# Optimization experiments

Measured on AMD Instinct MI355X. Metric: run time of the kernel, lower is better.

The kernel has to match this reference:

```python
import jax, jax.numpy as jnp
import numpy as np

N_NODES = 50000
N_EDGES = 800000
IN_DIM = 128
HID_DIM = 64
OUT_DIM = 40
N_REL = 8


def setup_inputs() -> dict:
    key = jax.random.key(0)
    ks = jax.random.split(key, 12)
    x = jax.random.normal(ks[0], (N_NODES, IN_DIM), dtype=jnp.float32)
    edge_index = jax.random.randint(ks[1], (2, N_EDGES), 0, N_NODES, dtype=jnp.int64)
    edge_type = jax.random.randint(ks[2], (N_EDGES,), 0, N_REL, dtype=jnp.int64)
    s = 0.05
    W1 = jax.random.normal(ks[3], (N_REL, IN_DIM, HID_DIM), dtype=jnp.float32) * s
    root1 = jax.random.normal(ks[4], (IN_DIM, HID_DIM), dtype=jnp.float32) * s
    b1 = jnp.zeros((HID_DIM,), dtype=jnp.float32)
    W2 = jax.random.normal(ks[5], (N_REL, HID_DIM, HID_DIM), dtype=jnp.float32) * s
    root2 = jax.random.normal(ks[6], (HID_DIM, HID_DIM), dtype=jnp.float32) * s
    b2 = jnp.zeros((HID_DIM,), dtype=jnp.float32)
    Wl = jax.random.normal(ks[7], (HID_DIM, OUT_DIM), dtype=jnp.float32) * s
    bl = jnp.zeros((OUT_DIM,), dtype=jnp.float32)
    return {"x": x, "edge_index": edge_index, "edge_type": edge_type,
            "W1": W1, "root1": root1, "b1": b1,
            "W2": W2, "root2": root2, "b2": b2,
            "Wl": Wl, "bl": bl}


def _rgcn_conv(x, W, Wroot, b, src, dst, edge_type):
    # PyG RGCNConv (no bases/blocks, aggr='mean'):
    #   out[i] = sum_r mean_{(j->i) of rel r} (x[j] @ W[r]) + x[i] @ Wroot + b
    N = x.shape[0]
    R = W.shape[0]
    h = jnp.einsum('ni,rio->rno', x, W)        # [R, N, out]
    msgs = h[edge_type, src]                   # [E, out] edge gather
    seg = edge_type * N + dst                  # per (relation, dst) segment
    sums = jax.ops.segment_sum(msgs, seg, num_segments=R * N)
    cnt = jax.ops.segment_sum(jnp.ones((msgs.shape[0],), x.dtype), seg,
                              num_segments=R * N)
    mean = sums / jnp.maximum(cnt, 1.0)[:, None]
    agg = mean.reshape(R, N, -1).sum(axis=0)   # sum over relations
    return agg + x @ Wroot + b


def reference(x, edge_index, edge_type, W1, root1, b1, W2, root2, b2, Wl, bl):
    src, dst = edge_index[0], edge_index[1]
    h = jax.nn.relu(_rgcn_conv(x, W1, root1, b1, src, dst, edge_type))
    # dropout is identity in eval mode
    h = jax.nn.relu(_rgcn_conv(h, W2, root2, b2, src, dst, edge_type))
    logits = h @ Wl + bl
    return jax.nn.log_softmax(logits, axis=1)
```

## Files before the change

kernel.cpp:

```cpp
#include <hip/hip_runtime.h>
#include <hip/hip_bf16.h>
#include <cmath>


#define IN_DIM 128
#define HID 64
#define OUT_DIM 40
#define NREL 8
#define NCOLS 576
#define CAP 64
#define CSTR 16

typedef __attribute__((ext_vector_type(8))) short short8;
typedef __attribute__((ext_vector_type(4))) short short4v;
typedef __attribute__((ext_vector_type(4))) float floatx4;
typedef __attribute__((ext_vector_type(2))) float f32x2;

static __device__ __forceinline__ short f2bf(float f) {
  __hip_bfloat16 h = __float2bfloat16(f);
  return __builtin_bit_cast(short, h);
}
static __device__ __forceinline__ float bflo(unsigned int u) {
  return __int_as_float(u << 16);
}
static __device__ __forceinline__ float bfhi(unsigned int u) {
  return __int_as_float(u & 0xffff0000u);
}
static __device__ __forceinline__ unsigned int packbf(float x, float y) {
  unsigned int lo = (unsigned short)f2bf(x);
  unsigned int hi = (unsigned short)f2bf(y);
  return lo | (hi << 16);
}

__global__ void pack_bt(const float* __restrict__ W1, const float* __restrict__ root1,
                        short* __restrict__ Bt1,
                        const float* __restrict__ W2, const float* __restrict__ root2,
                        short* __restrict__ Bt2,
                        int* __restrict__ cursor, int nzero4) {
  const int PB1 = (NCOLS * IN_DIM + 255) / 256;
  const int PB2 = (NCOLS * HID + 255) / 256;
  int b = blockIdx.x;
  if (b < PB1) {
    int i = b * 256 + threadIdx.x;
    if (i >= NCOLS * IN_DIM) return;
    int c = i / IN_DIM, k = i % IN_DIM;
    float v = (c < NREL * HID)
      ? W1[((size_t)(c >> 6) * IN_DIM + k) * HID + (c & 63)]
      : root1[(size_t)k * HID + (c - NREL * HID)];
    Bt1[i] = f2bf(v);
  } else if (b < PB1 + PB2) {
    int i = (b - PB1) * 256 + threadIdx.x;
    if (i >= NCOLS * HID) return;
    int c = i / HID, k = i % HID;
    float v = (c < NREL * HID)
      ? W2[((size_t)(c >> 6) * HID + k) * HID + (c & 63)]
      : root2[(size_t)k * HID + (c - NREL * HID)];
    Bt2[i] = f2bf(v);
  } else {
    int i = (b - PB1 - PB2) * 256 + threadIdx.x;
    if (i < nzero4) {
      int4 z; z.x = 0; z.y = 0; z.z = 0; z.w = 0;
      ((int4*)cursor)[i] = z;
    }
  }
}

template<int K, int AMODE>
__device__ __forceinline__ void gemm_dev(
    short* As, short* Bs,
    const void* __restrict__ Aptr, const short* __restrict__ Bt,
    const float* __restrict__ bias, short* __restrict__ H,
    unsigned short* __restrict__ AGG, int M, int row0)
{
  constexpr int AST = K + 8;
  int tid = threadIdx.x;
  int wv = tid >> 6, lane = tid & 63;
  int lm = lane & 15, quad = lane >> 4;

  if (AMODE == 0) {
    const float* A = (const float*)Aptr;
    constexpr int CH = K / 4;
    for (int i = tid; i < 64 * CH; i += 256) {
      int r = i / CH, kq = i % CH;
      int gr = row0 + r; if (gr >= M) gr = M - 1;
      float4 v = *(const float4*)(A + (unsigned)(gr * K + kq * 4));
      short4v s;
      s.x = f2bf(v.x); s.y = f2bf(v.y); s.z = f2bf(v.z); s.w = f2bf(v.w);
      *(short4v*)(As + r * AST + kq * 4) = s;
    }
  } else {
    const short* A = (const short*)Aptr;
    constexpr int CH = K / 8;
    for (int i = tid; i < 64 * CH; i += 256) {
      int r = i / CH, ko = i % CH;
      int gr = row0 + r; if (gr >= M) gr = M - 1;
      short8 v = *(const short8*)(A + (unsigned)(gr * K + ko * 8));
      #pragma unroll
      for (int j = 0; j < 8; ++j)
        if ((unsigned short)v[j] & 0x8000u) v[j] = 0;
      *(short8*)(As + r * AST + ko * 8) = v;
    }
  }

  const short* ap = As + (16 * wv + lm) * AST + quad * 8;

  for (int cy = 0; cy < 9; ++cy) {
    constexpr int CB = K / 8;
    for (int i = tid; i < 64 * CB; i += 256) {
      int n = i / CB, ko = i % CB;
      short8 v = *(const short8*)(Bt + (unsigned)((cy * 64 + n) * K + ko * 8));
      *(short8*)(Bs + n * AST + ko * 8) = v;
    }
    __syncthreads();

    floatx4 acc[4] = {{0,0,0,0},{0,0,0,0},{0,0,0,0},{0,0,0,0}};
    #pragma unroll
    for (int ks = 0; ks < K / 32; ++ks) {
      short8 a = *(const short8*)(ap + ks * 32);
      #pragma unroll
      for (int nb = 0; nb < 4; ++nb) {
        short8 b = *(const short8*)(Bs + (nb * 16 + lm) * AST + ks * 32 + quad * 8);
        acc[nb] = __builtin_amdgcn_mfma_f32_16x16x32_bf16(a, b, acc[nb], 0, 0, 0);
      }
    }
    __syncthreads();

    int mbase = row0 + 16 * wv + quad * 4;
    if (cy < 8) {
      #pragma unroll
      for (int nb = 0; nb < 4; ++nb) {
        int col = cy * 64 + nb * 16 + lm;
        #pragma unroll
        for (int r = 0; r < 4; ++r) {
          int mg = mbase + r;
          if (mg < M) H[(unsigned)mg * (NREL * HID) + col] = f2bf(acc[nb][r]);
        }
      }
    } else {
      #pragma unroll
      for (int nb = 0; nb < 4; ++nb) {
        int col = nb * 16 + lm;
        float bv = bias[col];
        #pragma unroll
        for (int r = 0; r < 4; ++r) {
          int mg = mbase + r;
          if (mg < M)
            AGG[(unsigned)mg * HID + col] = (unsigned short)f2bf(acc[nb][r] + bv);
        }
      }
    }
  }
}

__global__ __launch_bounds__(256, 4) void gemm1_scatter(
    const float* __restrict__ A, const short* __restrict__ Bt,
    const float* __restrict__ bias, short* __restrict__ H,
    unsigned short* __restrict__ AGG, int M, int GB,
    const int* __restrict__ src, const int* __restrict__ dst,
    const int* __restrict__ et,
    int* __restrict__ cursor, int* __restrict__ ev, int E)
{
  constexpr int AST = IN_DIM + 8;
  __shared__ short As[64 * AST];
  __shared__ short Bs[64 * AST];
  if ((int)blockIdx.x < GB) {
    gemm_dev<IN_DIM, 0>(As, Bs, A, Bt, bias, H, AGG, M, blockIdx.x * 64);
  } else {
    int e = (blockIdx.x - GB) * 256 + threadIdx.x;
    if (e >= E) return;
    int d = dst[e];
    int pos = atomicAdd(&cursor[d * CSTR], 1);
    if (pos < CAP)
      __builtin_nontemporal_store((src[e] << 3) | et[e], &ev[d * CAP + pos]);
  }
}

__global__ __launch_bounds__(256, 4) void gemm2_mfma(
    const unsigned short* __restrict__ A, const short* __restrict__ Bt,
    const float* __restrict__ bias, short* __restrict__ H,
    unsigned short* __restrict__ AGG, int M)
{
  constexpr int AST = HID + 8;
  __shared__ short As[64 * AST];
  __shared__ short Bs[64 * AST];
  gemm_dev<HID, 1>(As, Bs, A, Bt, bias, H, AGG, M, blockIdx.x * 64);
}

static __device__ __forceinline__ void agg_half2(
    const uint2* __restrict__ Hu2, const int* __restrict__ evrow,
    int cnt, int qloc, int sub, float wreg, int h,
    float& a0, float& a1, float& a2, float& a3)
{
  int npass = (cnt + 15) >> 4;
  f32x2 A01 = {a0, a1}, A23 = {a2, a3};
  for (int P = 0; P < npass; ++P) {
    const int4* pp = (const int4*)(evrow + P * 16 + qloc * 8);
    int4 v0 = pp[0], v1 = pp[1];
    int vv[8] = {v0.x, v0.y, v0.z, v0.w, v1.x, v1.y, v1.z, v1.w};
    int sb = P * 16 + qloc * 8;
    uint2 hv[8];
    float ww[8];
    #pragma unroll
    for (int i = 0; i < 8; ++i) {
      bool ok = (sb + i) < cnt;
      int v = ok ? vv[i] : 0;
      hv[i] = Hu2[(unsigned)v * 16u + (unsigned)sub];
      float w = __shfl(wreg, h * 32 + (v & 7), 64);
      ww[i] = ok ? w : 0.f;
    }
    #pragma unroll
    for (int i = 0; i < 8; ++i) {
      f32x2 w2 = {ww[i], ww[i]};
      f32x2 h01 = {bflo(hv[i].x), bfhi(hv[i].x)};
      f32x2 h23 = {bflo(hv[i].y), bfhi(hv[i].y)};
      A01 += h01 * w2;
      A23 += h23 * w2;
    }
  }
  a0 = A01.x; a1 = A01.y; a2 = A23.x; a3 = A23.y;
  a0 += __shfl_xor(a0, 16, 64);
  a1 += __shfl_xor(a1, 16, 64);
  a2 += __shfl_xor(a2, 16, 64);
  a3 += __shfl_xor(a3, 16, 64);
}

static __device__ __forceinline__ float rel_weight(
    const int* __restrict__ evr, int cnt, int lhl, int h)
{
  int e0 = evr[lhl], e1 = evr[lhl + 32];
  bool v0 = lhl < cnt, v1 = (lhl + 32) < cnt;
  int r0 = e0 & 7, r1 = e1 & 7;
  unsigned long long hm = 0xffffffffull << (h * 32);
  int myrel = lhl & 7;
  int c = 0;
  #pragma unroll
  for (int r = 0; r < 8; ++r) {
    unsigned long long m0 = __ballot(v0 && (r0 == r));
    unsigned long long m1 = __ballot(v1 && (r1 == r));
    int cr = __popcll(m0 & hm) + __popcll(m1 & hm);
    if (myrel == r) c = cr;
  }
  return (c > 0) ? (1.0f / (float)c) : 0.0f;
}

__global__ __launch_bounds__(256) void csr_agg(
    const short* __restrict__ H, const int* __restrict__ cursor,
    const int* __restrict__ ev, unsigned short* __restrict__ AGG, int N)
{
  int tid = threadIdx.x;
  int wv = tid >> 6, lane = tid & 63;
  int h = lane >> 5, lhl = lane & 31, qloc = lhl >> 4, sub = lhl & 15;
  int d = blockIdx.x * 8 + wv * 2 + h;
  int dc = d < N ? d : N - 1;

  int cnt = cursor[dc * CSTR]; if (cnt > CAP) cnt = CAP;
  const int* evr = ev + dc * CAP;
  float wreg = rel_weight(evr, cnt, lhl, h);

  float a0 = 0.f, a1 = 0.f, a2 = 0.f, a3 = 0.f;
  uint2* aggrow = (uint2*)(AGG + (size_t)dc * HID);
  if (qloc == 0) {
    uint2 iv = aggrow[sub];
    a0 = bflo(iv.x); a1 = bfhi(iv.x); a2 = bflo(iv.y); a3 = bfhi(iv.y);
  }
  agg_half2((const uint2*)H, evr, cnt, qloc, sub, wreg, h, a0, a1, a2, a3);
  if (d < N && qloc == 0) {
    uint2 ov;
    ov.x = packbf(a0, a1);
    ov.y = packbf(a2, a3);
    aggrow[sub] = ov;
  }
}

__global__ __launch_bounds__(256) void csr_agg_final(
    const short* __restrict__ H, const int* __restrict__ cursor,
    const int* __restrict__ ev, const unsigned short* __restrict__ AGG,
    const float* __restrict__ Wl, const float* __restrict__ bl,
    float* __restrict__ out, int N)
{
  __shared__ float sWl[HID * OUT_DIM];
  __shared__ float sbl[OUT_DIM];
  __shared__ float sh[8][HID];
  int tid = threadIdx.x;
  int wv = tid >> 6, lane = tid & 63;
  int h = lane >> 5, lhl = lane & 31, qloc = lhl >> 4, sub = lhl & 15;
  int d = blockIdx.x * 8 + wv * 2 + h;
  int dc = d < N ? d : N - 1;

  int cnt = cursor[dc * CSTR]; if (cnt > CAP) cnt = CAP;
  uint2 iv = ((const uint2*)(AGG + (size_t)dc * HID))[sub];
  const int* evr = ev + dc * CAP;
  float wreg = rel_weight(evr, cnt, lhl, h);

  for (int i = tid; i < HID * OUT_DIM; i += 256) sWl[i] = Wl[i];
  if (tid < OUT_DIM) sbl[tid] = bl[tid];
  __syncthreads();

  float a0 = 0.f, a1 = 0.f, a2 = 0.f, a3 = 0.f;
  if (qloc == 0) {
    a0 = bflo(iv.x); a1 = bfhi(iv.x); a2 = bflo(iv.y); a3 = bfhi(iv.y);
  }
  agg_half2((const uint2*)H, evr, cnt, qloc, sub, wreg, h, a0, a1, a2, a3);
  if (qloc == 0) {
    float4 v;
    v.x = fmaxf(a0, 0.f); v.y = fmaxf(a1, 0.f);
    v.z = fmaxf(a2, 0.f); v.w = fmaxf(a3, 0.f);
    *(float4*)(&sh[wv * 2 + h][4 * sub]) = v;
  }
  __syncthreads();

  #pragma unroll
  for (int ii = 0; ii < 2; ++ii) {
    int dd = blockIdx.x * 8 + wv * 2 + ii;
    const float* row = sh[wv * 2 + ii];
    float logit = -__builtin_inff();
    if (lane < OUT_DIM) {
      float t = sbl[lane];
      #pragma unroll 8
      for (int k = 0; k < HID; ++k) t += row[k] * sWl[k * OUT_DIM + lane];
      logit = t;
    }
    float m = logit;
    #pragma unroll
    for (int o = 32; o > 0; o >>= 1) m = fmaxf(m, __shfl_xor(m, o, 64));
    float ex = (lane < OUT_DIM) ? expf(logit - m) : 0.f;
    float s = ex;
    #pragma unroll
    for (int o = 32; o > 0; o >>= 1) s += __shfl_xor(s, o, 64);
    if (dd < N && lane < OUT_DIM)
      out[(size_t)dd * OUT_DIM + lane] = logit - m - logf(s);
  }
}

extern "C" void kernel_launch(void* const* d_in, const int* in_sizes, int n_in,
                              void* d_out, int out_size, void* d_ws, size_t ws_size,
                              hipStream_t stream) {
  const float* x     = (const float*)d_in[0];
  const int*   eidx  = (const int*)d_in[1];
  const int*   etype = (const int*)d_in[2];
  const float* W1    = (const float*)d_in[3];
  const float* root1 = (const float*)d_in[4];
  const float* b1    = (const float*)d_in[5];
  const float* W2    = (const float*)d_in[6];
  const float* root2 = (const float*)d_in[7];
  const float* b2    = (const float*)d_in[8];
  const float* Wl    = (const float*)d_in[9];
  const float* bl    = (const float*)d_in[10];

  int N = in_sizes[0] / IN_DIM;
  int E = in_sizes[2];
  const int* srcp = eidx;
  const int* dstp = eidx + E;

  char* ws = (char*)d_ws;
  size_t off = 0;
  auto alloc = [&](size_t bytes) -> char* {
    char* p = ws + off;
    off += (bytes + 255) & ~(size_t)255;
    return p;
  };
  short* Bt1    = (short*)alloc((size_t)NCOLS * IN_DIM * 2);
  short* Bt2    = (short*)alloc((size_t)NCOLS * HID * 2);
  int*   cursor = (int*)alloc((size_t)N * CSTR * 4);
  int*   ev     = (int*)alloc((size_t)N * CAP * 4);
  short* H1     = (short*)alloc((size_t)N * NREL * HID * 2);
  short* H2     = (short*)alloc((size_t)N * NREL * HID * 2);
  unsigned short* AGG1 = (unsigned short*)alloc((size_t)N * HID * 2);
  unsigned short* AGG2 = (unsigned short*)alloc((size_t)N * HID * 2);

  const int PB1 = (NCOLS * IN_DIM + 255) / 256;
  const int PB2 = (NCOLS * HID + 255) / 256;
  int nzero4 = (N * CSTR) / 4;
  int ZB = (nzero4 + 255) / 256;
  pack_bt<<<PB1 + PB2 + ZB, 256, 0, stream>>>(W1, root1, Bt1, W2, root2, Bt2,
                                              cursor, nzero4);

  int GB = (N + 63) / 64;
  int SB = (E + 255) / 256;
  gemm1_scatter<<<GB + SB, 256, 0, stream>>>(x, Bt1, b1, H1, AGG1, N, GB,
                                             srcp, dstp, etype, cursor, ev, E);

  csr_agg<<<(N + 7) / 8, 256, 0, stream>>>(H1, cursor, ev, AGG1, N);

  gemm2_mfma<<<GB, 256, 0, stream>>>(AGG1, Bt2, b2, H2, AGG2, N);

  csr_agg_final<<<(N + 7) / 8, 256, 0, stream>>>(H2, cursor, ev, AGG2,
                                                 Wl, bl, (float*)d_out, N);
}
```

Before: 217.1 us.

## Prefetch B tiles into registers, vectorize GEMM stores, split scatter kernel

```diff
diff --git a/kernel.cpp b/kernel.cpp
--- a/kernel.cpp
+++ b/kernel.cpp
@@ -65,6 +65,19 @@
   }
 }
 
+__global__ __launch_bounds__(256) void scatter_ev(
+    const int* __restrict__ src, const int* __restrict__ dst,
+    const int* __restrict__ et,
+    int* __restrict__ cursor, int* __restrict__ ev, int E)
+{
+  int e = blockIdx.x * 256 + threadIdx.x;
+  if (e >= E) return;
+  int d = dst[e];
+  int pos = atomicAdd(&cursor[d * CSTR], 1);
+  if (pos < CAP)
+    __builtin_nontemporal_store((src[e] << 3) | et[e], &ev[d * CAP + pos]);
+}
+
 template<int K, int AMODE>
 __device__ __forceinline__ void gemm_dev(
     short* As, short* Bs,
@@ -73,9 +86,23 @@
     unsigned short* __restrict__ AGG, int M, int row0)
 {
   constexpr int AST = K + 8;
+  constexpr int CB = K / 8;
+  constexpr int NCH = 64 * CB / 256;
   int tid = threadIdx.x;
   int wv = tid >> 6, lane = tid & 63;
   int lm = lane & 15, quad = lane >> 4;
+
+  int bn[NCH], bko[NCH];
+  #pragma unroll
+  for (int j = 0; j < NCH; ++j) {
+    int i = tid + j * 256;
+    bn[j] = i / CB; bko[j] = i % CB;
+  }
+
+  short8 breg[NCH];
+  #pragma unroll
+  for (int j = 0; j < NCH; ++j)
+    breg[j] = *(const short8*)(Bt + (unsigned)(bn[j] * K + bko[j] * 8));
 
   if (AMODE == 0) {
     const float* A = (const float*)Aptr;
@@ -103,15 +130,20 @@
   }
 
   const short* ap = As + (16 * wv + lm) * AST + quad * 8;
+  int rowg = row0 + 16 * wv + lm;
 
   for (int cy = 0; cy < 9; ++cy) {
-    constexpr int CB = K / 8;
-    for (int i = tid; i < 64 * CB; i += 256) {
-      int n = i / CB, ko = i % CB;
-      short8 v = *(const short8*)(Bt + (unsigned)((cy * 64 + n) * K + ko * 8));
-      *(short8*)(Bs + n * AST + ko * 8) = v;
-    }
+    #pragma unroll
+    for (int j = 0; j < NCH; ++j)
+      *(short8*)(Bs + bn[j] * AST + bko[j] * 8) = breg[j];
     __syncthreads();
+
+    if (cy < 8) {
+      #pragma unroll
+      for (int j = 0; j < NCH; ++j)
+        breg[j] = *(const short8*)(
+            Bt + (unsigned)(((cy + 1) * 64 + bn[j]) * K + bko[j] * 8));
+    }
 
     floatx4 acc[4] = {{0,0,0,0},{0,0,0,0},{0,0,0,0},{0,0,0,0}};
     #pragma unroll
@@ -120,59 +152,47 @@
       #pragma unroll
       for (int nb = 0; nb < 4; ++nb) {
         short8 b = *(const short8*)(Bs + (nb * 16 + lm) * AST + ks * 32 + quad * 8);
-        acc[nb] = __builtin_amdgcn_mfma_f32_16x16x32_bf16(a, b, acc[nb], 0, 0, 0);
+        acc[nb] = __builtin_amdgcn_mfma_f32_16x16x32_bf16(b, a, acc[nb], 0, 0, 0);
       }
     }
     __syncthreads();
 
-    int mbase = row0 + 16 * wv + quad * 4;
     if (cy < 8) {
-      #pragma unroll
-      for (int nb = 0; nb < 4; ++nb) {
-        int col = cy * 64 + nb * 16 + lm;
+      if (rowg < M) {
+        short* hrow = H + (unsigned)rowg * (NREL * HID) + cy * 64 + quad * 4;
         #pragma unroll
-        for (int r = 0; r < 4; ++r) {
-          int mg = mbase + r;
-          if (mg < M) H[(unsigned)mg * (NREL * HID) + col] = f2bf(acc[nb][r]);
+        for (int nb = 0; nb < 4; ++nb) {
+          short4v s;
+          s.x = f2bf(acc[nb][0]); s.y = f2bf(acc[nb][1]);
+          s.z = f2bf(acc[nb][2]); s.w = f2bf(acc[nb][3]);
+          *(short4v*)(hrow + nb * 16) = s;
         }
       }
     } else {
-      #pragma unroll
-      for (int nb = 0; nb < 4; ++nb) {
-        int col = nb * 16 + lm;
-        float bv = bias[col];
+      if (rowg < M) {
+        unsigned short* arow = AGG + (unsigned)rowg * HID + quad * 4;
         #pragma unroll
-        for (int r = 0; r < 4; ++r) {
-          int mg = mbase + r;
-          if (mg < M)
-            AGG[(unsigned)mg * HID + col] = (unsigned short)f2bf(acc[nb][r] + bv);
+        for (int nb = 0; nb < 4; ++nb) {
+          float4 bv = *(const float4*)(bias + nb * 16 + quad * 4);
+          short4v s;
+          s.x = f2bf(acc[nb][0] + bv.x); s.y = f2bf(acc[nb][1] + bv.y);
+          s.z = f2bf(acc[nb][2] + bv.z); s.w = f2bf(acc[nb][3] + bv.w);
+          *(short4v*)(arow + nb * 16) = s;
         }
       }
     }
   }
 }
 
-__global__ __launch_bounds__(256, 4) void gemm1_scatter(
+__global__ __launch_bounds__(256, 4) void gemm1_mfma(
     const float* __restrict__ A, const short* __restrict__ Bt,
     const float* __restrict__ bias, short* __restrict__ H,
-    unsigned short* __restrict__ AGG, int M, int GB,
-    const int* __restrict__ src, const int* __restrict__ dst,
-    const int* __restrict__ et,
-    int* __restrict__ cursor, int* __restrict__ ev, int E)
+    unsigned short* __restrict__ AGG, int M)
 {
   constexpr int AST = IN_DIM + 8;
   __shared__ short As[64 * AST];
   __shared__ short Bs[64 * AST];
-  if ((int)blockIdx.x < GB) {
-    gemm_dev<IN_DIM, 0>(As, Bs, A, Bt, bias, H, AGG, M, blockIdx.x * 64);
-  } else {
-    int e = (blockIdx.x - GB) * 256 + threadIdx.x;
-    if (e >= E) return;
-    int d = dst[e];
-    int pos = atomicAdd(&cursor[d * CSTR], 1);
-    if (pos < CAP)
-      __builtin_nontemporal_store((src[e] << 3) | et[e], &ev[d * CAP + pos]);
-  }
+  gemm_dev<IN_DIM, 0>(As, Bs, A, Bt, bias, H, AGG, M, blockIdx.x * 64);
 }
 
 __global__ __launch_bounds__(256, 4) void gemm2_mfma(
@@ -377,8 +397,9 @@
 
   int GB = (N + 63) / 64;
   int SB = (E + 255) / 256;
-  gemm1_scatter<<<GB + SB, 256, 0, stream>>>(x, Bt1, b1, H1, AGG1, N, GB,
-                                             srcp, dstp, etype, cursor, ev, E);
+  scatter_ev<<<SB, 256, 0, stream>>>(srcp, dstp, etype, cursor, ev, E);
+
+  gemm1_mfma<<<GB, 256, 0, stream>>>(x, Bt1, b1, H1, AGG1, N);
 
   csr_agg<<<(N + 7) / 8, 256, 0, stream>>>(H1, cursor, ev, AGG1, N);
 
```

Result: slower. 258.8 us (+19.2%).

## Aggregate-then-transform layer 2 with per-relation edge buckets

Applied to the files above, without the earlier changes.

```diff
diff --git a/kernel.cpp b/kernel.cpp
--- a/kernel.cpp
+++ b/kernel.cpp
@@ -8,13 +8,14 @@
 #define OUT_DIM 40
 #define NREL 8
 #define NCOLS 576
-#define CAP 64
+#define K2 576
+#define CAPR 32
+#define EVR 256
 #define CSTR 16
 
 typedef __attribute__((ext_vector_type(8))) short short8;
 typedef __attribute__((ext_vector_type(4))) short short4v;
 typedef __attribute__((ext_vector_type(4))) float floatx4;
-typedef __attribute__((ext_vector_type(2))) float f32x2;
 
 static __device__ __forceinline__ short f2bf(float f) {
   __hip_bfloat16 h = __float2bfloat16(f);
@@ -35,10 +36,10 @@
 __global__ void pack_bt(const float* __restrict__ W1, const float* __restrict__ root1,
                         short* __restrict__ Bt1,
                         const float* __restrict__ W2, const float* __restrict__ root2,
-                        short* __restrict__ Bt2,
+                        short* __restrict__ Bt2b,
                         int* __restrict__ cursor, int nzero4) {
   const int PB1 = (NCOLS * IN_DIM + 255) / 256;
-  const int PB2 = (NCOLS * HID + 255) / 256;
+  const int PB2 = (64 * K2 + 255) / 256;
   int b = blockIdx.x;
   if (b < PB1) {
     int i = b * 256 + threadIdx.x;
@@ -50,12 +51,12 @@
     Bt1[i] = f2bf(v);
   } else if (b < PB1 + PB2) {
     int i = (b - PB1) * 256 + threadIdx.x;
-    if (i >= NCOLS * HID) return;
-    int c = i / HID, k = i % HID;
-    float v = (c < NREL * HID)
-      ? W2[((size_t)(c >> 6) * HID + k) * HID + (c & 63)]
-      : root2[(size_t)k * HID + (c - NREL * HID)];
-    Bt2[i] = f2bf(v);
+    if (i >= 64 * K2) return;
+    int col = i / K2, kk = i % K2;
+    float v = (kk < NREL * HID)
+      ? W2[(size_t)kk * HID + col]
+      : root2[(size_t)(kk - NREL * HID) * HID + col];
+    Bt2b[i] = f2bf(v);
   } else {
     int i = (b - PB1 - PB2) * 256 + threadIdx.x;
     if (i < nzero4) {
@@ -65,20 +66,19 @@
   }
 }
 
-template<int K, int AMODE>
-__device__ __forceinline__ void gemm_dev(
+__device__ __forceinline__ void gemm1_body(
     short* As, short* Bs,
-    const void* __restrict__ Aptr, const short* __restrict__ Bt,
+    const float* __restrict__ A, const short* __restrict__ Bt,
     const float* __restrict__ bias, short* __restrict__ H,
     unsigned short* __restrict__ AGG, int M, int row0)
 {
+  constexpr int K = IN_DIM;
   constexpr int AST = K + 8;
   int tid = threadIdx.x;
   int wv = tid >> 6, lane = tid & 63;
   int lm = lane & 15, quad = lane >> 4;
 
-  if (AMODE == 0) {
-    const float* A = (const float*)Aptr;
+  {
     constexpr int CH = K / 4;
     for (int i = tid; i < 64 * CH; i += 256) {
       int r = i / CH, kq = i % CH;
@@ -87,18 +87,6 @@
       short4v s;
       s.x = f2bf(v.x); s.y = f2bf(v.y); s.z = f2bf(v.z); s.w = f2bf(v.w);
       *(short4v*)(As + r * AST + kq * 4) = s;
-    }
-  } else {
-    const short* A = (const short*)Aptr;
-    constexpr int CH = K / 8;
-    for (int i = tid; i < 64 * CH; i += 256) {
-      int r = i / CH, ko = i % CH;
-      int gr = row0 + r; if (gr >= M) gr = M - 1;
-      short8 v = *(const short8*)(A + (unsigned)(gr * K + ko * 8));
-      #pragma unroll
-      for (int j = 0; j < 8; ++j)
-        if ((unsigned short)v[j] & 0x8000u) v[j] = 0;
-      *(short8*)(As + r * AST + ko * 8) = v;
     }
   }
 
@@ -164,160 +152,163 @@
   __shared__ short As[64 * AST];
   __shared__ short Bs[64 * AST];
   if ((int)blockIdx.x < GB) {
-    gemm_dev<IN_DIM, 0>(As, Bs, A, Bt, bias, H, AGG, M, blockIdx.x * 64);
+    gemm1_body(As, Bs, A, Bt, bias, H, AGG, M, blockIdx.x * 64);
   } else {
     int e = (blockIdx.x - GB) * 256 + threadIdx.x;
     if (e >= E) return;
     int d = dst[e];
-    int pos = atomicAdd(&cursor[d * CSTR], 1);
-    if (pos < CAP)
-      __builtin_nontemporal_store((src[e] << 3) | et[e], &ev[d * CAP + pos]);
-  }
-}
-
-__global__ __launch_bounds__(256, 4) void gemm2_mfma(
-    const unsigned short* __restrict__ A, const short* __restrict__ Bt,
-    const float* __restrict__ bias, short* __restrict__ H,
-    unsigned short* __restrict__ AGG, int M)
-{
-  constexpr int AST = HID + 8;
+    int r = et[e];
+    int pos = atomicAdd(&cursor[d * CSTR + r], 1);
+    if (pos < CAPR)
+      __builtin_nontemporal_store(src[e], &ev[(d << 8) + (r << 5) + pos]);
+  }
+}
+
+__global__ __launch_bounds__(256) void csr_agg1(
+    const short* __restrict__ H1, const int* __restrict__ cursor,
+    const int* __restrict__ ev, unsigned short* __restrict__ h, int N)
+{
+  int tid = threadIdx.x;
+  int wv = tid >> 6, lane = tid & 63;
+  int rel = lane >> 3, dg = lane & 7;
+  int d = blockIdx.x * 4 + wv;
+
+  int cnt = cursor[d * CSTR + rel]; if (cnt > CAPR) cnt = CAPR;
+  const int* evg = ev + ((size_t)d << 8) + (rel << 5);
+  int evs = evg[dg];
+
+  float acc[8] = {0.f,0.f,0.f,0.f,0.f,0.f,0.f,0.f};
+  for (int s = 0; s < cnt; ++s) {
+    int srcj = (s < 8) ? __shfl(evs, (lane & 56) + s, 64) : evg[s];
+    uint4 hv = *(const uint4*)(H1 + ((size_t)srcj << 9) + (rel << 6) + (dg << 3));
+    acc[0] += bflo(hv.x); acc[1] += bfhi(hv.x);
+    acc[2] += bflo(hv.y); acc[3] += bfhi(hv.y);
+    acc[4] += bflo(hv.z); acc[5] += bfhi(hv.z);
+    acc[6] += bflo(hv.w); acc[7] += bfhi(hv.w);
+  }
+  float w = (cnt > 0) ? (1.0f / (float)cnt) : 0.0f;
+  #pragma unroll
+  for (int j = 0; j < 8; ++j) acc[j] *= w;
+  #pragma unroll
+  for (int off = 8; off <= 32; off <<= 1) {
+    #pragma unroll
+    for (int j = 0; j < 8; ++j) acc[j] += __shfl_xor(acc[j], off, 64);
+  }
+  if (rel == 0) {
+    unsigned short* hrow = h + (size_t)d * HID + (dg << 3);
+    uint4 sv = *(const uint4*)hrow;
+    float v0 = fmaxf(acc[0] + bflo(sv.x), 0.f);
+    float v1 = fmaxf(acc[1] + bfhi(sv.x), 0.f);
+    float v2 = fmaxf(acc[2] + bflo(sv.y), 0.f);
+    float v3 = fmaxf(acc[3] + bfhi(sv.y), 0.f);
+    float v4 = fmaxf(acc[4] + bflo(sv.z), 0.f);
+    float v5 = fmaxf(acc[5] + bfhi(sv.z), 0.f);
+    float v6 = fmaxf(acc[6] + bflo(sv.w), 0.f);
+    float v7 = fmaxf(acc[7] + bfhi(sv.w), 0.f);
+    uint4 ov;
+    ov.x = packbf(v0, v1); ov.y = packbf(v2, v3);
+    ov.z = packbf(v4, v5); ov.w = packbf(v6, v7);
+    *(uint4*)hrow = ov;
+  }
+}
+
+__global__ __launch_bounds__(256) void agg2(
+    const unsigned short* __restrict__ h, const int* __restrict__ cursor,
+    const int* __restrict__ ev, short* __restrict__ m2, int N)
+{
+  int tid = threadIdx.x;
+  int wv = tid >> 6, lane = tid & 63;
+  int rel = lane >> 3, dg = lane & 7;
+  int d = blockIdx.x * 4 + wv;
+
+  int cnt = cursor[d * CSTR + rel]; if (cnt > CAPR) cnt = CAPR;
+  const int* evg = ev + ((size_t)d << 8) + (rel << 5);
+  int evs = evg[dg];
+
+  float acc[8] = {0.f,0.f,0.f,0.f,0.f,0.f,0.f,0.f};
+  for (int s = 0; s < cnt; ++s) {
+    int srcj = (s < 8) ? __shfl(evs, (lane & 56) + s, 64) : evg[s];
+    uint4 hv = *(const uint4*)(h + ((size_t)srcj << 6) + (dg << 3));
+    acc[0] += bflo(hv.x); acc[1] += bfhi(hv.x);
+    acc[2] += bflo(hv.y); acc[3] += bfhi(hv.y);
+    acc[4] += bflo(hv.z); acc[5] += bfhi(hv.z);
+    acc[6] += bflo(hv.w); acc[7] += bfhi(hv.w);
+  }
+  float w = (cnt > 0) ? (1.0f / (float)cnt) : 0.0f;
+  uint4 ov;
+  ov.x = packbf(acc[0] * w, acc[1] * w);
+  ov.y = packbf(acc[2] * w, acc[3] * w);
+  ov.z = packbf(acc[4] * w, acc[5] * w);
+  ov.w = packbf(acc[6] * w, acc[7] * w);
+  *(uint4*)(m2 + (size_t)d * K2 + (rel << 6) + (dg << 3)) = ov;
+  if (rel == 0) {
+    uint4 hv = *(const uint4*)(h + ((size_t)d << 6) + (dg << 3));
+    *(uint4*)(m2 + (size_t)d * K2 + 512 + (dg << 3)) = hv;
+  }
+}
+
+__global__ __launch_bounds__(256) void gemm2c(
+    const short* __restrict__ m2, const short* __restrict__ Bt2b,
+    const float* __restrict__ b2, const float* __restrict__ Wl,
+    const float* __restrict__ bl, float* __restrict__ out, int N)
+{
+  constexpr int AST = 64 + 8;
   __shared__ short As[64 * AST];
   __shared__ short Bs[64 * AST];
-  gemm_dev<HID, 1>(As, Bs, A, Bt, bias, H, AGG, M, blockIdx.x * 64);
-}
-
-static __device__ __forceinline__ void agg_half2(
-    const uint2* __restrict__ Hu2, const int* __restrict__ evrow,
-    int cnt, int qloc, int sub, float wreg, int h,
-    float& a0, float& a1, float& a2, float& a3)
-{
-  int npass = (cnt + 15) >> 4;
-  f32x2 A01 = {a0, a1}, A23 = {a2, a3};
-  for (int P = 0; P < npass; ++P) {
-    const int4* pp = (const int4*)(evrow + P * 16 + qloc * 8);
-    int4 v0 = pp[0], v1 = pp[1];
-    int vv[8] = {v0.x, v0.y, v0.z, v0.w, v1.x, v1.y, v1.z, v1.w};
-    int sb = P * 16 + qloc * 8;
-    uint2 hv[8];
-    float ww[8];
-    #pragma unroll
-    for (int i = 0; i < 8; ++i) {
-      bool ok = (sb + i) < cnt;
-      int v = ok ? vv[i] : 0;
-      hv[i] = Hu2[(unsigned)v * 16u + (unsigned)sub];
-      float w = __shfl(wreg, h * 32 + (v & 7), 64);
-      ww[i] = ok ? w : 0.f;
-    }
-    #pragma unroll
-    for (int i = 0; i < 8; ++i) {
-      f32x2 w2 = {ww[i], ww[i]};
-      f32x2 h01 = {bflo(hv[i].x), bfhi(hv[i].x)};
-      f32x2 h23 = {bflo(hv[i].y), bfhi(hv[i].y)};
-      A01 += h01 * w2;
-      A23 += h23 * w2;
-    }
-  }
-  a0 = A01.x; a1 = A01.y; a2 = A23.x; a3 = A23.y;
-  a0 += __shfl_xor(a0, 16, 64);
-  a1 += __shfl_xor(a1, 16, 64);
-  a2 += __shfl_xor(a2, 16, 64);
-  a3 += __shfl_xor(a3, 16, 64);
-}
-
-static __device__ __forceinline__ float rel_weight(
-    const int* __restrict__ evr, int cnt, int lhl, int h)
-{
-  int e0 = evr[lhl], e1 = evr[lhl + 32];
-  bool v0 = lhl < cnt, v1 = (lhl + 32) < cnt;
-  int r0 = e0 & 7, r1 = e1 & 7;
-  unsigned long long hm = 0xffffffffull << (h * 32);
-  int myrel = lhl & 7;
-  int c = 0;
-  #pragma unroll
-  for (int r = 0; r < 8; ++r) {
-    unsigned long long m0 = __ballot(v0 && (r0 == r));
-    unsigned long long m1 = __ballot(v1 && (r1 == r));
-    int cr = __popcll(m0 & hm) + __popcll(m1 & hm);
-    if (myrel == r) c = cr;
-  }
-  return (c > 0) ? (1.0f / (float)c) : 0.0f;
-}
-
-__global__ __launch_bounds__(256) void csr_agg(
-    const short* __restrict__ H, const int* __restrict__ cursor,
-    const int* __restrict__ ev, unsigned short* __restrict__ AGG, int N)
-{
+  __shared__ float sz[64][64];
+  __shared__ float sWl[HID * OUT_DIM];
+  __shared__ float sbl[OUT_DIM];
   int tid = threadIdx.x;
   int wv = tid >> 6, lane = tid & 63;
-  int h = lane >> 5, lhl = lane & 31, qloc = lhl >> 4, sub = lhl & 15;
-  int d = blockIdx.x * 8 + wv * 2 + h;
-  int dc = d < N ? d : N - 1;
-
-  int cnt = cursor[dc * CSTR]; if (cnt > CAP) cnt = CAP;
-  const int* evr = ev + dc * CAP;
-  float wreg = rel_weight(evr, cnt, lhl, h);
-
-  float a0 = 0.f, a1 = 0.f, a2 = 0.f, a3 = 0.f;
-  uint2* aggrow = (uint2*)(AGG + (size_t)dc * HID);
-  if (qloc == 0) {
-    uint2 iv = aggrow[sub];
-    a0 = bflo(iv.x); a1 = bfhi(iv.x); a2 = bflo(iv.y); a3 = bfhi(iv.y);
-  }
-  agg_half2((const uint2*)H, evr, cnt, qloc, sub, wreg, h, a0, a1, a2, a3);
-  if (d < N && qloc == 0) {
-    uint2 ov;
-    ov.x = packbf(a0, a1);
-    ov.y = packbf(a2, a3);
-    aggrow[sub] = ov;
-  }
-}
-
-__global__ __launch_bounds__(256) void csr_agg_final(
-    const short* __restrict__ H, const int* __restrict__ cursor,
-    const int* __restrict__ ev, const unsigned short* __restrict__ AGG,
-    const float* __restrict__ Wl, const float* __restrict__ bl,
-    float* __restrict__ out, int N)
-{
-  __shared__ float sWl[HID * OUT_DIM];
-  __shared__ float sbl[OUT_DIM];
-  __shared__ float sh[8][HID];
-  int tid = threadIdx.x;
-  int wv = tid >> 6, lane = tid & 63;
-  int h = lane >> 5, lhl = lane & 31, qloc = lhl >> 4, sub = lhl & 15;
-  int d = blockIdx.x * 8 + wv * 2 + h;
-  int dc = d < N ? d : N - 1;
-
-  int cnt = cursor[dc * CSTR]; if (cnt > CAP) cnt = CAP;
-  uint2 iv = ((const uint2*)(AGG + (size_t)dc * HID))[sub];
-  const int* evr = ev + dc * CAP;
-  float wreg = rel_weight(evr, cnt, lhl, h);
+  int lm = lane & 15, quad = lane >> 4;
+  int row0 = blockIdx.x * 64;
 
   for (int i = tid; i < HID * OUT_DIM; i += 256) sWl[i] = Wl[i];
   if (tid < OUT_DIM) sbl[tid] = bl[tid];
-  __syncthreads();
-
-  float a0 = 0.f, a1 = 0.f, a2 = 0.f, a3 = 0.f;
-  if (qloc == 0) {
-    a0 = bflo(iv.x); a1 = bfhi(iv.x); a2 = bflo(iv.y); a3 = bfhi(iv.y);
-  }
-  agg_half2((const uint2*)H, evr, cnt, qloc, sub, wreg, h, a0, a1, a2, a3);
-  if (qloc == 0) {
-    float4 v;
-    v.x = fmaxf(a0, 0.f); v.y = fmaxf(a1, 0.f);
-    v.z = fmaxf(a2, 0.f); v.w = fmaxf(a3, 0.f);
-    *(float4*)(&sh[wv * 2 + h][4 * sub]) = v;
-  }
-  __syncthreads();
+
+  floatx4 acc[4] = {{0,0,0,0},{0,0,0,0},{0,0,0,0},{0,0,0,0}};
+  for (int kt = 0; kt < 9; ++kt) {
+    #pragma unroll
+    for (int j = 0; j < 2; ++j) {
+      int i = tid + j * 256;
+      int r = i >> 3, ch = i & 7;
+      int gr = row0 + r; if (gr >= N) gr = N - 1;
+      *(short8*)(As + r * AST + ch * 8) =
+          *(const short8*)(m2 + (size_t)gr * K2 + kt * 64 + ch * 8);
+      *(short8*)(Bs + r * AST + ch * 8) =
+          *(const short8*)(Bt2b + (unsigned)(r * K2 + kt * 64 + ch * 8));
+    }
+    __syncthreads();
+    #pragma unroll
+    for (int ks = 0; ks < 2; ++ks) {
+      short8 a = *(const short8*)(As + (16 * wv + lm) * AST + ks * 32 + quad * 8);
+      #pragma unroll
+      for (int nb = 0; nb < 4; ++nb) {
+        short8 b = *(const short8*)(Bs + (nb * 16 + lm) * AST + ks * 32 + quad * 8);
+        acc[nb] = __builtin_amdgcn_mfma_f32_16x16x32_bf16(a, b, acc[nb], 0, 0, 0);
+      }
+    }
+    __syncthreads();
+  }
 
   #pragma unroll
-  for (int ii = 0; ii < 2; ++ii) {
-    int dd = blockIdx.x * 8 + wv * 2 + ii;
-    const float* row = sh[wv * 2 + ii];
+  for (int nb = 0; nb < 4; ++nb) {
+    int col = nb * 16 + lm;
+    float bv = b2[col];
+    #pragma unroll
+    for (int r = 0; r < 4; ++r)
+      sz[16 * wv + quad * 4 + r][col] = fmaxf(acc[nb][r] + bv, 0.f);
+  }
+
+  for (int rr = 0; rr < 16; ++rr) {
+    int row = 16 * wv + rr;
+    int dd = row0 + row;
+    const float* zr = sz[row];
     float logit = -__builtin_inff();
     if (lane < OUT_DIM) {
       float t = sbl[lane];
       #pragma unroll 8
-      for (int k = 0; k < HID; ++k) t += row[k] * sWl[k * OUT_DIM + lane];
+      for (int k = 0; k < HID; ++k) t += zr[k] * sWl[k * OUT_DIM + lane];
       logit = t;
     }
     float m = logit;
@@ -360,19 +351,19 @@
     return p;
   };
   short* Bt1    = (short*)alloc((size_t)NCOLS * IN_DIM * 2);
-  short* Bt2    = (short*)alloc((size_t)NCOLS * HID * 2);
+  short* Bt2b   = (short*)alloc((size_t)64 * K2 * 2);
   int*   cursor = (int*)alloc((size_t)N * CSTR * 4);
-  int*   ev     = (int*)alloc((size_t)N * CAP * 4);
-  short* H1     = (short*)alloc((size_t)N * NREL * HID * 2);
-  short* H2     = (short*)alloc((size_t)N * NREL * HID * 2);
+  int*   ev     = (int*)alloc((size_t)N * EVR * 4);
+  char*  h1m2   = alloc((size_t)N * K2 * 2);
+  short* H1     = (short*)h1m2;
+  short* m2     = (short*)h1m2;
   unsigned short* AGG1 = (unsigned short*)alloc((size_t)N * HID * 2);
-  unsigned short* AGG2 = (unsigned short*)alloc((size_t)N * HID * 2);
 
   const int PB1 = (NCOLS * IN_DIM + 255) / 256;
-  const int PB2 = (NCOLS * HID + 255) / 256;
+  const int PB2 = (64 * K2 + 255) / 256;
   int nzero4 = (N * CSTR) / 4;
   int ZB = (nzero4 + 255) / 256;
-  pack_bt<<<PB1 + PB2 + ZB, 256, 0, stream>>>(W1, root1, Bt1, W2, root2, Bt2,
+  pack_bt<<<PB1 + PB2 + ZB, 256, 0, stream>>>(W1, root1, Bt1, W2, root2, Bt2b,
                                               cursor, nzero4);
 
   int GB = (N + 63) / 64;
@@ -380,10 +371,9 @@
   gemm1_scatter<<<GB + SB, 256, 0, stream>>>(x, Bt1, b1, H1, AGG1, N, GB,
                                              srcp, dstp, etype, cursor, ev, E);
 
-  csr_agg<<<(N + 7) / 8, 256, 0, stream>>>(H1, cursor, ev, AGG1, N);
-
-  gemm2_mfma<<<GB, 256, 0, stream>>>(AGG1, Bt2, b2, H2, AGG2, N);
-
-  csr_agg_final<<<(N + 7) / 8, 256, 0, stream>>>(H2, cursor, ev, AGG2,
-                                                 Wl, bl, (float*)d_out, N);
-}
+  csr_agg1<<<N / 4, 256, 0, stream>>>(H1, cursor, ev, AGG1, N);
+
+  agg2<<<N / 4, 256, 0, stream>>>(AGG1, cursor, ev, m2, N);
+
+  gemm2c<<<GB, 256, 0, stream>>>(m2, Bt2b, b2, Wl, bl, (float*)d_out, N);
+}
```

After: 263.0 us. 21.2% more time.
